# Optimization experiments

Measured on AMD Instinct MI355X. Metric: run time of the kernel, lower is better.

## Reference

```python
import jax, jax.numpy as jnp
import numpy as np

N, D, E, EDGE_DIM, HID4 = 8192, 128, 262144, 50, 32


def setup_inputs() -> dict:
    key = jax.random.key(0)
    k = jax.random.split(key, 8)
    return {
        "mag": jax.random.uniform(k[0], (N, D), dtype=jnp.float32),
        "phase": jax.random.normal(k[1], (N, D), dtype=jnp.float32),
        "edge_index": jax.random.randint(k[2], (2, E), 0, N, dtype=jnp.int64),
        "rbf": jax.random.uniform(k[3], (E, EDGE_DIM), dtype=jnp.float32),
        "W1": jax.random.normal(k[4], (EDGE_DIM, HID4), dtype=jnp.float32) * 0.1,
        "b1": jnp.zeros((HID4,), dtype=jnp.float32),
        "W2": jax.random.normal(k[5], (HID4, 1), dtype=jnp.float32) * 0.1,
        "b2": jnp.zeros((1,), dtype=jnp.float32),
    }


def reference(mag, phase, edge_index, rbf, W1, b1, W2, b2):
    # score_ij = sum_d |z_i||z_j| cos(theta_i - theta_j) / sqrt(D)
    # cos(a-b) identity: = (mag*cos(phase)) @ (mag*cos(phase))^T + (mag*sin)@(mag*sin)^T
    scale = jnp.sqrt(jnp.asarray(mag.shape[-1], mag.dtype))
    a = mag * jnp.cos(phase)  # [N, D]
    b = mag * jnp.sin(phase)  # [N, D]
    scores = (a @ a.T + b @ b.T) / scale  # [N, N]
    # edge bias: Linear -> SiLU -> Linear -> scalar, scattered onto (i, j)
    h = jax.nn.silu(rbf @ W1 + b1)       # [E, HID4]
    bias = (h @ W2 + b2)[:, 0]           # [E]
    scores = scores.at[edge_index[0], edge_index[1]].add(bias)
    attn = jax.nn.softmax(scores, axis=1)  # softmax over keys j
    new_mag = attn @ mag
    new_phase = attn @ phase
    return new_mag, new_phase
```

## Files before the change

### kernel.cpp

```cpp
#include <hip/hip_runtime.h>
#include <hip/hip_bf16.h>

#define NN 8192
#define DD 128
#define DQK 256
#define EE 262144
#define EDGE_DIM 50
#define HID 32
#define CAP 96
#define SCALE 0.08838834764831845f
#define SCALE_LOG2E 0.12752455522410585f

using f32x4 = __attribute__((ext_vector_type(4))) float;
using f32x2 = __attribute__((ext_vector_type(2))) float;
using bf16x8 = __attribute__((ext_vector_type(8))) short;
using s16x4 = __attribute__((ext_vector_type(4))) short;

static __device__ __forceinline__ short f2b(float f) {
  __hip_bfloat16 h = __float2bfloat16(f);
  return __builtin_bit_cast(short, h);
}
static __device__ __forceinline__ float b2f(short s) {
  unsigned u = ((unsigned)(unsigned short)s) << 16;
  return __builtin_bit_cast(float, u);
}
static __device__ __forceinline__ void gll(const short* g, short* l) {
  __builtin_amdgcn_global_load_lds(
      (const __attribute__((address_space(1))) void*)g,
      (__attribute__((address_space(3))) void*)l, 16, 0, 0);
}

__global__ __launch_bounds__(256) void k1_mega(
    const float* __restrict__ mag, const float* __restrict__ phase,
    short* __restrict__ qkb, short* __restrict__ vtb,
    const float* __restrict__ rbf, const float* __restrict__ W1,
    const float* __restrict__ b1, const float* __restrict__ W2,
    const float* __restrict__ b2, const int* __restrict__ eidx,
    float* __restrict__ bias, int* __restrict__ cnt, int* __restrict__ slot) {
  __shared__ float tile[64][65];
  __shared__ alignas(16) float w1s[EDGE_DIM * HID];
  __shared__ alignas(16) float b1s[HID];
  __shared__ alignas(16) float w2s[HID];
  __shared__ float b2s;
  int b = blockIdx.x;
  int tid = threadIdx.x;
  if (b < 4096) {
    int t = b * 256 + tid;
    int n = t >> 7, d = t & 127;
    float m = mag[t], p = phase[t];
    float sn, cs;
    __sincosf(p, &sn, &cs);
    qkb[(size_t)n * DQK + d] = f2b(m * cs);
    qkb[(size_t)n * DQK + 128 + d] = f2b(m * sn);
    return;
  }
  if (b < 4608) {
    int r = b - 4096;
    int bn = r & 127, bd = (r >> 7) & 1, sel = r >> 8;
    const float* src = sel ? phase : mag;
#pragma unroll
    for (int rep = 0; rep < 16; ++rep) {
      int idx = rep * 256 + tid;
      int rr = idx >> 6, c = idx & 63;
      tile[rr][c] = src[(size_t)(bn * 64 + rr) * DD + bd * 64 + c];
    }
    __syncthreads();
#pragma unroll
    for (int rep = 0; rep < 16; ++rep) {
      int idx = rep * 256 + tid;
      int rr = idx >> 6, c = idx & 63;
      vtb[(size_t)(sel * 128 + bd * 64 + rr) * NN + bn * 64 + c] = f2b(tile[c][rr]);
    }
    return;
  }
  for (int k = tid; k < EDGE_DIM * HID; k += 256) w1s[k] = W1[k];
  if (tid < HID) { b1s[tid] = b1[tid]; w2s[tid] = W2[tid]; }
  if (tid == 0) b2s = b2[0];
  __syncthreads();
  int e = (b - 4608) * 256 + tid;
  const float* rrow = rbf + (size_t)e * EDGE_DIM;
  f32x4 r4[12];
#pragma unroll
  for (int k = 0; k < 12; ++k) r4[k] = *reinterpret_cast<const f32x4*>(rrow + 4 * k);
  f32x2 rt2 = *reinterpret_cast<const f32x2*>(rrow + 48);
  f32x4 h[8];
#pragma unroll
  for (int jj = 0; jj < 8; ++jj) h[jj] = reinterpret_cast<const f32x4*>(b1s)[jj];
#pragma unroll
  for (int k = 0; k < 12; ++k) {
#pragma unroll
    for (int qq = 0; qq < 4; ++qq) {
      const f32x4* wrow = reinterpret_cast<const f32x4*>(w1s + (4 * k + qq) * HID);
#pragma unroll
      for (int jj = 0; jj < 8; ++jj) h[jj] += r4[k][qq] * wrow[jj];
    }
  }
  {
    const f32x4* w48 = reinterpret_cast<const f32x4*>(w1s + 48 * HID);
    const f32x4* w49 = reinterpret_cast<const f32x4*>(w1s + 49 * HID);
#pragma unroll
    for (int jj = 0; jj < 8; ++jj) h[jj] += rt2.x * w48[jj] + rt2.y * w49[jj];
  }
  float outv = b2s;
#pragma unroll
  for (int jj = 0; jj < 8; ++jj) {
    f32x4 x = h[jj];
    f32x4 sl;
#pragma unroll
    for (int q = 0; q < 4; ++q) sl[q] = x[q] / (1.0f + __expf(-x[q]));
    f32x4 pr = sl * reinterpret_cast<const f32x4*>(w2s)[jj];
    outv += pr.x + pr.y + pr.z + pr.w;
  }
  bias[e] = outv;
  int i = eidx[e];
  int p = atomicAdd(&cnt[i], 1);
  if (p < CAP) slot[i * CAP + p] = e;
}

constexpr int TBM = 64;
constexpr int TBN = 128;

template <int NSPLIT>
__global__ __launch_bounds__(512, 4) void k5_flash(
    const short* __restrict__ qk,
    const short* __restrict__ vt,
    float* __restrict__ nump,
    float* __restrict__ denp) {
  constexpr int QCOLS = NN / NSPLIT;
  constexpr int NCHUNK = QCOLS / TBN;
  constexpr int GPQ = 8 / NSPLIT;
  __shared__ alignas(16) short Qs[TBM * 256];
  __shared__ alignas(16) short KV[2 * TBN * 64];
  __shared__ alignas(16) short Ps[TBM * 128];
  int b = blockIdx.x;
  int q = (b & 7) / GPQ;
  int rb = (b >> 3) * GPQ + (b & (GPQ - 1));
  int tid = threadIdx.x;
  int w = tid >> 6, lane = tid & 63;
  int wr = w >> 2, wc = w & 3;
  int l15 = lane & 15, quad = lane >> 4;
  int rsw = l15 & 7;
  int wbase = w * 64;
  int r0 = rb * TBM;
  int cbase = q * QCOLS;

#pragma unroll
  for (int p = 0; p < 4; ++p) {
    int idx = p * 512 + tid;
    int row = idx >> 5, gs = idx & 31;
    gll(qk + (size_t)(r0 + row) * DQK + ((gs ^ (row & 7)) * 8),
        &Qs[(p * 512 + wbase) * 8]);
  }

  f32x4 o[2][4] = {};
  float den[2][4] = {};
  __syncthreads();

  for (int ch = 0; ch < NCHUNK; ++ch) {
    int c0 = cbase + ch * TBN;
#pragma unroll
    for (int p = 0; p < 2; ++p) {
      int idx = p * 512 + tid;
      int col = idx >> 3, gs = idx & 7;
      gll(qk + (size_t)(c0 + col) * DQK + ((gs ^ (col & 7)) * 8),
          &KV[(p * 512 + wbase) * 8]);
    }
    __syncthreads();
    f32x4 s[2][2] = {};
#pragma unroll
    for (int bk = 0; bk < 4; ++bk) {
      int buf = bk & 1;
      if (bk < 3) {
        int nb = buf ^ 1;
#pragma unroll
        for (int p = 0; p < 2; ++p) {
          int idx = p * 512 + tid;
          int col = idx >> 3, gs = idx & 7;
          gll(qk + (size_t)(c0 + col) * DQK + (bk + 1) * 64 + ((gs ^ (col & 7)) * 8),
              &KV[nb * 8192 + (p * 512 + wbase) * 8]);
        }
      }
#pragma unroll
      for (int ks = 0; ks < 2; ++ks) {
        int g = ks * 4 + quad;
        bf16x8 a[2], bb[2];
#pragma unroll
        for (int rt = 0; rt < 2; ++rt)
          a[rt] = *(const bf16x8*)&Qs[(wr * 32 + rt * 16 + l15) * 256 +
                                      ((bk * 8 + g) ^ rsw) * 8];
#pragma unroll
        for (int ct = 0; ct < 2; ++ct)
          bb[ct] = *(const bf16x8*)&KV[buf * 8192 + (wc * 32 + ct * 16 + l15) * 64 +
                                       (g ^ rsw) * 8];
#pragma unroll
        for (int rt = 0; rt < 2; ++rt)
#pragma unroll
          for (int ct = 0; ct < 2; ++ct)
            s[rt][ct] = __builtin_amdgcn_mfma_f32_16x16x32_bf16(a[rt], bb[ct],
                                                                s[rt][ct], 0, 0, 0);
      }
      __syncthreads();
    }
#pragma unroll
    for (int rt = 0; rt < 2; ++rt)
#pragma unroll
      for (int ct = 0; ct < 2; ++ct) {
        int col = wc * 32 + ct * 16 + l15;
        int cg = col >> 3, co = col & 7;
#pragma unroll
        for (int r = 0; r < 4; ++r) {
          float pv = exp2f(s[rt][ct][r] * SCALE_LOG2E);
          den[rt][r] += pv;
          int row = wr * 32 + rt * 16 + quad * 4 + r;
          Ps[row * 128 + ((cg ^ (row & 7)) * 8 + co)] = f2b(pv);
        }
      }
    __syncthreads();
#pragma unroll
    for (int jb = 0; jb < 2; ++jb) {
#pragma unroll
      for (int p = 0; p < 4; ++p) {
        int idx = p * 512 + tid;
        int feat = idx >> 3, gs = idx & 7;
        gll(vt + (size_t)feat * NN + c0 + jb * 64 + ((gs ^ (feat & 7)) * 8),
            &KV[(p * 512 + wbase) * 8]);
      }
      __syncthreads();
#pragma unroll
      for (int ks = 0; ks < 2; ++ks) {
        int g = ks * 4 + quad;
        bf16x8 pa[2], vb[4];
#pragma unroll
        for (int rt = 0; rt < 2; ++rt) {
          int row = wr * 32 + rt * 16 + l15;
          pa[rt] = *(const bf16x8*)&Ps[row * 128 +
                                       (((jb * 8 + g) ^ (row & 7)) * 8)];
        }
#pragma unroll
        for (int ft = 0; ft < 4; ++ft)
          vb[ft] = *(const bf16x8*)&KV[(wc * 64 + ft * 16 + l15) * 64 + (g ^ rsw) * 8];
#pragma unroll
        for (int rt = 0; rt < 2; ++rt)
#pragma unroll
          for (int ft = 0; ft < 4; ++ft)
            o[rt][ft] = __builtin_amdgcn_mfma_f32_16x16x32_bf16(pa[rt], vb[ft],
                                                                o[rt][ft], 0, 0, 0);
      }
      __syncthreads();
    }
  }
  float* npB = nump + (size_t)q * NN * DQK;
#pragma unroll
  for (int rt = 0; rt < 2; ++rt)
#pragma unroll
    for (int ft = 0; ft < 4; ++ft) {
      int row = r0 + wr * 32 + rt * 16 + quad * 4;
      int feat = wc * 64 + ft * 16 + l15;
#pragma unroll
      for (int r = 0; r < 4; ++r)
        npB[(size_t)(row + r) * DQK + feat] = o[rt][ft][r];
    }
  float* dl = reinterpret_cast<float*>(KV);
#pragma unroll
  for (int rt = 0; rt < 2; ++rt)
#pragma unroll
    for (int r = 0; r < 4; ++r) {
      float d = den[rt][r];
      d += __shfl_xor(d, 1);
      d += __shfl_xor(d, 2);
      d += __shfl_xor(d, 4);
      d += __shfl_xor(d, 8);
      if (l15 == 0) dl[wc * TBM + wr * 32 + rt * 16 + quad * 4 + r] = d;
    }
  __syncthreads();
  if (tid < TBM) {
    float d = dl[0 * TBM + tid] + dl[1 * TBM + tid] + dl[2 * TBM + tid] +
              dl[3 * TBM + tid];
    denp[q * NN + r0 + tid] = d;
  }
}

__global__ __launch_bounds__(256) void k6_combine(
    const int* __restrict__ eidx, const float* __restrict__ bias,
    const int* __restrict__ cntArr, const int* __restrict__ slot,
    const short* __restrict__ qk, const float* __restrict__ mag,
    const float* __restrict__ phase, const float* __restrict__ nump,
    const float* __restrict__ denp, float* __restrict__ out, int nsplit) {
  __shared__ short qs[DQK];
  __shared__ int js[CAP];
  __shared__ float bs[CAP];
  __shared__ float ess[CAP];
  __shared__ int keepf[CAP];
  __shared__ f32x4 ncl[4][64];
  __shared__ float dcl[4];
  int i = blockIdx.x;
  int tid = threadIdx.x;
  int wave = tid >> 6;
  int lane = tid & 63;
  int cnt = cntArr[i];
  if (cnt > CAP) cnt = CAP;
  if (tid < DQK) qs[tid] = qk[(size_t)i * DQK + tid];
  for (int p = tid; p < cnt; p += 256) {
    int e = slot[i * CAP + p];
    js[p] = eidx[EE + e];
    bs[p] = bias[e];
  }
  __syncthreads();
  int sub = lane & 7;
  for (int p = wave * 8 + (lane >> 3); p < cnt; p += 32) {
    int j = js[p];
    const bf16x8* kb = reinterpret_cast<const bf16x8*>(qk + (size_t)j * DQK + sub * 32);
    const bf16x8* qa = reinterpret_cast<const bf16x8*>(qs + sub * 32);
    float sp = 0.f;
#pragma unroll
    for (int t = 0; t < 4; ++t) {
      bf16x8 qv = qa[t];
      bf16x8 kv = kb[t];
#pragma unroll
      for (int u = 0; u < 8; ++u) sp += b2f(qv[u]) * b2f(kv[u]);
    }
    sp += __shfl_xor(sp, 1);
    sp += __shfl_xor(sp, 2);
    sp += __shfl_xor(sp, 4);
    if (sub == 0) ess[p] = __expf(sp * SCALE);
  }
  __syncthreads();
  {
    float bsum = 0.f;
    int keep = 0;
    if (tid < cnt) {
      int j = js[tid];
      bsum = bs[tid];
      keep = 1;
      for (int qq = 0; qq < cnt; ++qq) {
        if (qq == tid || js[qq] != j) continue;
        if (qq < tid) { keep = 0; break; }
        bsum += bs[qq];
      }
    }
    __syncthreads();
    if (tid < cnt) { bs[tid] = bsum; keepf[tid] = keep; }
    __syncthreads();
  }
  const float* vbase = (lane < 32) ? (mag + 4 * lane) : (phase + 4 * lane - 128);
  f32x4 nc = {0.f, 0.f, 0.f, 0.f};
  float denc = 0.f;
  if (wave < nsplit) {
    nc = *reinterpret_cast<const f32x4*>(nump + ((size_t)wave * NN + i) * DQK + 4 * lane);
    if (lane == 0) denc = denp[wave * NN + i];
  }
  for (int p = wave; p < cnt; p += 4) {
    if (!keepf[p]) continue;
    float delta = ess[p] * expm1f(bs[p]);
    denc += delta;
    f32x4 v = *reinterpret_cast<const f32x4*>(vbase + (size_t)js[p] * DD);
    nc += delta * v;
  }
  ncl[wave][lane] = nc;
  if (lane == 0) dcl[wave] = denc;
  __syncthreads();
  if (wave == 0) {
    f32x4 nd = ncl[0][lane] + ncl[1][lane] + ncl[2][lane] + ncl[3][lane];
    float den = dcl[0] + dcl[1] + dcl[2] + dcl[3];
    f32x4 res = nd * (1.0f / den);
    if (lane < 32)
      *reinterpret_cast<f32x4*>(out + (size_t)i * DD + 4 * lane) = res;
    else
      *reinterpret_cast<f32x4*>(out + (size_t)NN * DD + (size_t)i * DD + 4 * lane - 128) = res;
  }
}

constexpr size_t OFF_QK = 0;
constexpr size_t OFF_VT = (size_t)NN * DQK * 2;
constexpr size_t OFF_BIAS = OFF_VT + (size_t)DQK * NN * 2;
constexpr size_t OFF_CNT = OFF_BIAS + (size_t)EE * 4;
constexpr size_t OFF_SLOT = OFF_CNT + (size_t)NN * 4;
constexpr size_t OFF_NUMP = (OFF_SLOT + (size_t)NN * CAP * 4 + 255) & ~(size_t)255;
constexpr size_t WS_NEED4 = OFF_NUMP + 4ull * NN * DQK * 4 + 4ull * NN * 4;
constexpr size_t WS_NEED2 = OFF_NUMP + 2ull * NN * DQK * 4 + 2ull * NN * 4;

extern "C" void kernel_launch(void* const* d_in, const int* in_sizes, int n_in,
                              void* d_out, int out_size, void* d_ws, size_t ws_size,
                              hipStream_t stream) {
  const float* mag = (const float*)d_in[0];
  const float* phase = (const float*)d_in[1];
  const int* eidx = (const int*)d_in[2];
  const float* rbf = (const float*)d_in[3];
  const float* W1 = (const float*)d_in[4];
  const float* b1 = (const float*)d_in[5];
  const float* W2 = (const float*)d_in[6];
  const float* b2 = (const float*)d_in[7];
  float* out = (float*)d_out;
  char* ws = (char*)d_ws;
  if (ws_size < WS_NEED2) return;
  int nsplit = (ws_size >= WS_NEED4) ? 4 : 2;

  short* qkb = (short*)(ws + OFF_QK);
  short* vtb = (short*)(ws + OFF_VT);
  float* bias = (float*)(ws + OFF_BIAS);
  int* cnt = (int*)(ws + OFF_CNT);
  int* slot = (int*)(ws + OFF_SLOT);
  float* nump = (float*)(ws + OFF_NUMP);
  float* denp = (float*)(ws + OFF_NUMP + (size_t)nsplit * NN * DQK * 4);

  hipMemsetAsync(cnt, 0, (size_t)NN * 4, stream);
  k1_mega<<<5632, 256, 0, stream>>>(mag, phase, qkb, vtb, rbf, W1, b1, W2, b2,
                                    eidx, bias, cnt, slot);
  if (nsplit == 4)
    k5_flash<4><<<(NN / TBM) * 4, 512, 0, stream>>>(qkb, vtb, nump, denp);
  else
    k5_flash<2><<<(NN / TBM) * 2, 512, 0, stream>>>(qkb, vtb, nump, denp);
  k6_combine<<<NN, 256, 0, stream>>>(eidx, bias, cnt, slot, qkb, mag, phase, nump,
                                     denp, out, nsplit);
}
```

Measured before the change: 292.8 us.

## Hold Q fragments in registers and load full K/V tiles per chunk

The flash kernel now keeps each wave's Q rows as register fragments instead of staging Q in shared memory. The wave grid changes from 2x4 to 4x2, so each wave owns 16 rows and 64 key columns (128 output features). Each chunk loads the whole 128x256 K tile, and then the whole V tile, into one shared buffer in a single pass, replacing the 4-step double-buffered K loads and the 2-step V loads. This cuts the number of barriers and LDS reads of Q. In exchange it gives up the overlap between K loads and MFMA work, raises register pressure from the qf and o arrays, and changes the LDS footprint, which may affect occupancy under launch_bounds(512,4).

New measurement: 420.2 us. +43.5%, slower.

```diff
diff --git a/kernel.cpp b/kernel.cpp
--- a/kernel.cpp
+++ b/kernel.cpp
@@ -129,155 +129,111 @@
   constexpr int QCOLS = NN / NSPLIT;
   constexpr int NCHUNK = QCOLS / TBN;
   constexpr int GPQ = 8 / NSPLIT;
-  __shared__ alignas(16) short Qs[TBM * 256];
-  __shared__ alignas(16) short KV[2 * TBN * 64];
+  __shared__ alignas(16) short Kb[TBN * 256];
   __shared__ alignas(16) short Ps[TBM * 128];
   int b = blockIdx.x;
   int q = (b & 7) / GPQ;
   int rb = (b >> 3) * GPQ + (b & (GPQ - 1));
   int tid = threadIdx.x;
   int w = tid >> 6, lane = tid & 63;
-  int wr = w >> 2, wc = w & 3;
+  int wr = w >> 1, wc = w & 1;
   int l15 = lane & 15, quad = lane >> 4;
-  int rsw = l15 & 7;
   int wbase = w * 64;
   int r0 = rb * TBM;
   int cbase = q * QCOLS;
 
-#pragma unroll
-  for (int p = 0; p < 4; ++p) {
-    int idx = p * 512 + tid;
-    int row = idx >> 5, gs = idx & 31;
-    gll(qk + (size_t)(r0 + row) * DQK + ((gs ^ (row & 7)) * 8),
-        &Qs[(p * 512 + wbase) * 8]);
-  }
-
-  f32x4 o[2][4] = {};
-  float den[2][4] = {};
-  __syncthreads();
+  bf16x8 qf[8];
+  {
+    const short* qrow = qk + (size_t)(r0 + wr * 16 + l15) * DQK;
+#pragma unroll
+    for (int ks = 0; ks < 8; ++ks)
+      qf[ks] = *(const bf16x8*)(qrow + ks * 32 + quad * 8);
+  }
+
+  f32x4 o[8] = {};
+  float den[4] = {};
 
   for (int ch = 0; ch < NCHUNK; ++ch) {
     int c0 = cbase + ch * TBN;
-#pragma unroll
-    for (int p = 0; p < 2; ++p) {
+    __syncthreads();
+#pragma unroll
+    for (int p = 0; p < 8; ++p) {
       int idx = p * 512 + tid;
-      int col = idx >> 3, gs = idx & 7;
+      int col = idx >> 5, gs = idx & 31;
       gll(qk + (size_t)(c0 + col) * DQK + ((gs ^ (col & 7)) * 8),
-          &KV[(p * 512 + wbase) * 8]);
-    }
-    __syncthreads();
-    f32x4 s[2][2] = {};
-#pragma unroll
-    for (int bk = 0; bk < 4; ++bk) {
-      int buf = bk & 1;
-      if (bk < 3) {
-        int nb = buf ^ 1;
-#pragma unroll
-        for (int p = 0; p < 2; ++p) {
-          int idx = p * 512 + tid;
-          int col = idx >> 3, gs = idx & 7;
-          gll(qk + (size_t)(c0 + col) * DQK + (bk + 1) * 64 + ((gs ^ (col & 7)) * 8),
-              &KV[nb * 8192 + (p * 512 + wbase) * 8]);
-        }
+          &Kb[(p * 512 + wbase) * 8]);
+    }
+    __syncthreads();
+    f32x4 s[4] = {};
+#pragma unroll
+    for (int ks = 0; ks < 8; ++ks) {
+      int g = ks * 4 + quad;
+      bf16x8 kf[4];
+#pragma unroll
+      for (int ct = 0; ct < 4; ++ct) {
+        int col = wc * 64 + ct * 16 + l15;
+        kf[ct] = *(const bf16x8*)&Kb[col * 256 + ((g ^ (col & 7)) * 8)];
       }
 #pragma unroll
-      for (int ks = 0; ks < 2; ++ks) {
-        int g = ks * 4 + quad;
-        bf16x8 a[2], bb[2];
-#pragma unroll
-        for (int rt = 0; rt < 2; ++rt)
-          a[rt] = *(const bf16x8*)&Qs[(wr * 32 + rt * 16 + l15) * 256 +
-                                      ((bk * 8 + g) ^ rsw) * 8];
-#pragma unroll
-        for (int ct = 0; ct < 2; ++ct)
-          bb[ct] = *(const bf16x8*)&KV[buf * 8192 + (wc * 32 + ct * 16 + l15) * 64 +
-                                       (g ^ rsw) * 8];
-#pragma unroll
-        for (int rt = 0; rt < 2; ++rt)
-#pragma unroll
-          for (int ct = 0; ct < 2; ++ct)
-            s[rt][ct] = __builtin_amdgcn_mfma_f32_16x16x32_bf16(a[rt], bb[ct],
-                                                                s[rt][ct], 0, 0, 0);
+      for (int ct = 0; ct < 4; ++ct)
+        s[ct] = __builtin_amdgcn_mfma_f32_16x16x32_bf16(qf[ks], kf[ct], s[ct], 0, 0, 0);
+    }
+#pragma unroll
+    for (int ct = 0; ct < 4; ++ct) {
+      int col = wc * 64 + ct * 16 + l15;
+      int cg = col >> 3, co = col & 7;
+#pragma unroll
+      for (int r = 0; r < 4; ++r) {
+        float pv = exp2f(s[ct][r] * SCALE_LOG2E);
+        den[r] += pv;
+        int row = wr * 16 + quad * 4 + r;
+        Ps[row * 128 + ((cg ^ (row & 7)) * 8 + co)] = f2b(pv);
       }
-      __syncthreads();
-    }
-#pragma unroll
-    for (int rt = 0; rt < 2; ++rt)
-#pragma unroll
-      for (int ct = 0; ct < 2; ++ct) {
-        int col = wc * 32 + ct * 16 + l15;
-        int cg = col >> 3, co = col & 7;
-#pragma unroll
-        for (int r = 0; r < 4; ++r) {
-          float pv = exp2f(s[rt][ct][r] * SCALE_LOG2E);
-          den[rt][r] += pv;
-          int row = wr * 32 + rt * 16 + quad * 4 + r;
-          Ps[row * 128 + ((cg ^ (row & 7)) * 8 + co)] = f2b(pv);
-        }
+    }
+    __syncthreads();
+#pragma unroll
+    for (int p = 0; p < 8; ++p) {
+      int idx = p * 512 + tid;
+      int feat = idx >> 4, gs = idx & 15;
+      gll(vt + (size_t)feat * NN + c0 + ((gs ^ (feat & 7)) * 8),
+          &Kb[(p * 512 + wbase) * 8]);
+    }
+    __syncthreads();
+#pragma unroll
+    for (int ks = 0; ks < 4; ++ks) {
+      int g = ks * 4 + quad;
+      int row = wr * 16 + l15;
+      bf16x8 pa = *(const bf16x8*)&Ps[row * 128 + ((g ^ (row & 7)) * 8)];
+#pragma unroll
+      for (int ft = 0; ft < 8; ++ft) {
+        int feat = wc * 128 + ft * 16 + l15;
+        bf16x8 vb = *(const bf16x8*)&Kb[feat * 128 + ((g ^ (feat & 7)) * 8)];
+        o[ft] = __builtin_amdgcn_mfma_f32_16x16x32_bf16(pa, vb, o[ft], 0, 0, 0);
       }
-    __syncthreads();
-#pragma unroll
-    for (int jb = 0; jb < 2; ++jb) {
-#pragma unroll
-      for (int p = 0; p < 4; ++p) {
-        int idx = p * 512 + tid;
-        int feat = idx >> 3, gs = idx & 7;
-        gll(vt + (size_t)feat * NN + c0 + jb * 64 + ((gs ^ (feat & 7)) * 8),
-            &KV[(p * 512 + wbase) * 8]);
-      }
-      __syncthreads();
-#pragma unroll
-      for (int ks = 0; ks < 2; ++ks) {
-        int g = ks * 4 + quad;
-        bf16x8 pa[2], vb[4];
-#pragma unroll
-        for (int rt = 0; rt < 2; ++rt) {
-          int row = wr * 32 + rt * 16 + l15;
-          pa[rt] = *(const bf16x8*)&Ps[row * 128 +
-                                       (((jb * 8 + g) ^ (row & 7)) * 8)];
-        }
-#pragma unroll
-        for (int ft = 0; ft < 4; ++ft)
-          vb[ft] = *(const bf16x8*)&KV[(wc * 64 + ft * 16 + l15) * 64 + (g ^ rsw) * 8];
-#pragma unroll
-        for (int rt = 0; rt < 2; ++rt)
-#pragma unroll
-          for (int ft = 0; ft < 4; ++ft)
-            o[rt][ft] = __builtin_amdgcn_mfma_f32_16x16x32_bf16(pa[rt], vb[ft],
-                                                                o[rt][ft], 0, 0, 0);
-      }
-      __syncthreads();
     }
   }
   float* npB = nump + (size_t)q * NN * DQK;
 #pragma unroll
-  for (int rt = 0; rt < 2; ++rt)
-#pragma unroll
-    for (int ft = 0; ft < 4; ++ft) {
-      int row = r0 + wr * 32 + rt * 16 + quad * 4;
-      int feat = wc * 64 + ft * 16 + l15;
-#pragma unroll
-      for (int r = 0; r < 4; ++r)
-        npB[(size_t)(row + r) * DQK + feat] = o[rt][ft][r];
-    }
-  float* dl = reinterpret_cast<float*>(KV);
-#pragma unroll
-  for (int rt = 0; rt < 2; ++rt)
-#pragma unroll
-    for (int r = 0; r < 4; ++r) {
-      float d = den[rt][r];
-      d += __shfl_xor(d, 1);
-      d += __shfl_xor(d, 2);
-      d += __shfl_xor(d, 4);
-      d += __shfl_xor(d, 8);
-      if (l15 == 0) dl[wc * TBM + wr * 32 + rt * 16 + quad * 4 + r] = d;
-    }
-  __syncthreads();
-  if (tid < TBM) {
-    float d = dl[0 * TBM + tid] + dl[1 * TBM + tid] + dl[2 * TBM + tid] +
-              dl[3 * TBM + tid];
-    denp[q * NN + r0 + tid] = d;
-  }
+  for (int ft = 0; ft < 8; ++ft) {
+    int row = r0 + wr * 16 + quad * 4;
+    int feat = wc * 128 + ft * 16 + l15;
+#pragma unroll
+    for (int r = 0; r < 4; ++r)
+      npB[(size_t)(row + r) * DQK + feat] = o[ft][r];
+  }
+  __syncthreads();
+  float* dl = reinterpret_cast<float*>(Kb);
+#pragma unroll
+  for (int r = 0; r < 4; ++r) {
+    float d = den[r];
+    d += __shfl_xor(d, 1);
+    d += __shfl_xor(d, 2);
+    d += __shfl_xor(d, 4);
+    d += __shfl_xor(d, 8);
+    if (l15 == 0) dl[wc * TBM + wr * 16 + quad * 4 + r] = d;
+  }
+  __syncthreads();
+  if (tid < TBM) denp[q * NN + r0 + tid] = dl[tid] + dl[TBM + tid];
 }
 
 __global__ __launch_bounds__(256) void k6_combine(
```

## Shrink combine kernel to one wave and gather bf16 values for edge corrections

Applied to the files above, without the earlier changes.

k1 now also writes a row-major bf16 copy of mag and phase, and k6_combine gathers its sparse edge-correction value rows from that copy instead of from the fp32 inputs, halving the bytes per gathered row. The combine kernel drops from 256 to 64 threads per row. It does all per-edge work in one wave with two half-wave groups and sums the split partials in the final step. This cuts block overhead and gather traffic, but adds a bf16 write in k1 and lowers precision of the correction term.

Measured after the change: 270.5 us. -7.6%, faster.

```diff
diff --git a/kernel.cpp b/kernel.cpp
--- a/kernel.cpp
+++ b/kernel.cpp
@@ -32,7 +32,7 @@
 
 __global__ __launch_bounds__(256) void k1_mega(
     const float* __restrict__ mag, const float* __restrict__ phase,
-    short* __restrict__ qkb, short* __restrict__ vtb,
+    short* __restrict__ qkb, short* __restrict__ vtb, short* __restrict__ vb16,
     const float* __restrict__ rbf, const float* __restrict__ W1,
     const float* __restrict__ b1, const float* __restrict__ W2,
     const float* __restrict__ b2, const int* __restrict__ eidx,
@@ -52,6 +52,8 @@
     __sincosf(p, &sn, &cs);
     qkb[(size_t)n * DQK + d] = f2b(m * cs);
     qkb[(size_t)n * DQK + 128 + d] = f2b(m * sn);
+    vb16[(size_t)n * DQK + d] = f2b(m);
+    vb16[(size_t)n * DQK + 128 + d] = f2b(p);
     return;
   }
   if (b < 4608) {
@@ -280,34 +282,33 @@
   }
 }
 
-__global__ __launch_bounds__(256) void k6_combine(
+__global__ __launch_bounds__(64) void k6_combine(
     const int* __restrict__ eidx, const float* __restrict__ bias,
     const int* __restrict__ cntArr, const int* __restrict__ slot,
-    const short* __restrict__ qk, const float* __restrict__ mag,
-    const float* __restrict__ phase, const float* __restrict__ nump,
-    const float* __restrict__ denp, float* __restrict__ out, int nsplit) {
+    const short* __restrict__ qk, const short* __restrict__ vb16,
+    const float* __restrict__ nump, const float* __restrict__ denp,
+    float* __restrict__ out, int nsplit) {
   __shared__ short qs[DQK];
   __shared__ int js[CAP];
   __shared__ float bs[CAP];
   __shared__ float ess[CAP];
   __shared__ int keepf[CAP];
-  __shared__ f32x4 ncl[4][64];
-  __shared__ float dcl[4];
+  __shared__ float ncl[2][32][8];
+  __shared__ float dcl[2];
   int i = blockIdx.x;
-  int tid = threadIdx.x;
-  int wave = tid >> 6;
-  int lane = tid & 63;
+  int lane = threadIdx.x;
   int cnt = cntArr[i];
   if (cnt > CAP) cnt = CAP;
-  if (tid < DQK) qs[tid] = qk[(size_t)i * DQK + tid];
-  for (int p = tid; p < cnt; p += 256) {
+  *reinterpret_cast<s16x4*>(&qs[lane * 4]) =
+      *reinterpret_cast<const s16x4*>(qk + (size_t)i * DQK + lane * 4);
+  for (int p = lane; p < cnt; p += 64) {
     int e = slot[i * CAP + p];
     js[p] = eidx[EE + e];
     bs[p] = bias[e];
   }
   __syncthreads();
   int sub = lane & 7;
-  for (int p = wave * 8 + (lane >> 3); p < cnt; p += 32) {
+  for (int p = lane >> 3; p < cnt; p += 8) {
     int j = js[p];
     const bf16x8* kb = reinterpret_cast<const bf16x8*>(qk + (size_t)j * DQK + sub * 32);
     const bf16x8* qa = reinterpret_cast<const bf16x8*>(qs + sub * 32);
@@ -326,53 +327,74 @@
   }
   __syncthreads();
   {
-    float bsum = 0.f;
-    int keep = 0;
-    if (tid < cnt) {
-      int j = js[tid];
-      bsum = bs[tid];
-      keep = 1;
+    int myp[2];
+    float mybsum[2];
+    int mykeep[2];
+    int nm = 0;
+    for (int p = lane; p < cnt; p += 64) {
+      int j = js[p];
+      float bsum = bs[p];
+      int keep = 1;
       for (int qq = 0; qq < cnt; ++qq) {
-        if (qq == tid || js[qq] != j) continue;
-        if (qq < tid) { keep = 0; break; }
+        if (qq == p || js[qq] != j) continue;
+        if (qq < p) { keep = 0; break; }
         bsum += bs[qq];
       }
+      myp[nm] = p; mybsum[nm] = bsum; mykeep[nm] = keep; ++nm;
     }
     __syncthreads();
-    if (tid < cnt) { bs[tid] = bsum; keepf[tid] = keep; }
+    for (int k = 0; k < nm; ++k) { bs[myp[k]] = mybsum[k]; keepf[myp[k]] = mykeep[k]; }
     __syncthreads();
   }
-  const float* vbase = (lane < 32) ? (mag + 4 * lane) : (phase + 4 * lane - 128);
-  f32x4 nc = {0.f, 0.f, 0.f, 0.f};
+  int grp = lane >> 5;
+  int l31 = lane & 31;
+  f32x4 nc0 = {0.f, 0.f, 0.f, 0.f}, nc1 = {0.f, 0.f, 0.f, 0.f};
   float denc = 0.f;
-  if (wave < nsplit) {
-    nc = *reinterpret_cast<const f32x4*>(nump + ((size_t)wave * NN + i) * DQK + 4 * lane);
-    if (lane == 0) denc = denp[wave * NN + i];
-  }
-  for (int p = wave; p < cnt; p += 4) {
+  for (int p = grp; p < cnt; p += 2) {
     if (!keepf[p]) continue;
     float delta = ess[p] * expm1f(bs[p]);
     denc += delta;
-    f32x4 v = *reinterpret_cast<const f32x4*>(vbase + (size_t)js[p] * DD);
-    nc += delta * v;
-  }
-  ncl[wave][lane] = nc;
-  if (lane == 0) dcl[wave] = denc;
-  __syncthreads();
-  if (wave == 0) {
-    f32x4 nd = ncl[0][lane] + ncl[1][lane] + ncl[2][lane] + ncl[3][lane];
-    float den = dcl[0] + dcl[1] + dcl[2] + dcl[3];
-    f32x4 res = nd * (1.0f / den);
-    if (lane < 32)
-      *reinterpret_cast<f32x4*>(out + (size_t)i * DD + 4 * lane) = res;
-    else
-      *reinterpret_cast<f32x4*>(out + (size_t)NN * DD + (size_t)i * DD + 4 * lane - 128) = res;
+    bf16x8 v = *reinterpret_cast<const bf16x8*>(vb16 + (size_t)js[p] * DQK + l31 * 8);
+#pragma unroll
+    for (int u = 0; u < 4; ++u) nc0[u] += delta * b2f(v[u]);
+#pragma unroll
+    for (int u = 0; u < 4; ++u) nc1[u] += delta * b2f(v[4 + u]);
+  }
+#pragma unroll
+  for (int u = 0; u < 4; ++u) {
+    ncl[grp][l31][u] = nc0[u];
+    ncl[grp][l31][4 + u] = nc1[u];
+  }
+  if (l31 == 0) dcl[grp] = denc;
+  __syncthreads();
+  if (grp == 0) {
+    float den = dcl[0] + dcl[1];
+    f32x4 a0, a1;
+#pragma unroll
+    for (int u = 0; u < 4; ++u) {
+      a0[u] = ncl[0][l31][u] + ncl[1][l31][u];
+      a1[u] = ncl[0][l31][4 + u] + ncl[1][l31][4 + u];
+    }
+    for (int qq = 0; qq < nsplit; ++qq) {
+      const float* np = nump + ((size_t)qq * NN + i) * DQK + l31 * 8;
+      a0 += *reinterpret_cast<const f32x4*>(np);
+      a1 += *reinterpret_cast<const f32x4*>(np + 4);
+      den += denp[qq * NN + i];
+    }
+    float inv = 1.0f / den;
+    a0 *= inv;
+    a1 *= inv;
+    float* dst = (l31 < 16) ? (out + (size_t)i * DD + l31 * 8)
+                            : (out + (size_t)NN * DD + (size_t)i * DD + l31 * 8 - 128);
+    *reinterpret_cast<f32x4*>(dst) = a0;
+    *reinterpret_cast<f32x4*>(dst + 4) = a1;
   }
 }
 
 constexpr size_t OFF_QK = 0;
 constexpr size_t OFF_VT = (size_t)NN * DQK * 2;
-constexpr size_t OFF_BIAS = OFF_VT + (size_t)DQK * NN * 2;
+constexpr size_t OFF_VB16 = OFF_VT + (size_t)DQK * NN * 2;
+constexpr size_t OFF_BIAS = OFF_VB16 + (size_t)NN * DQK * 2;
 constexpr size_t OFF_CNT = OFF_BIAS + (size_t)EE * 4;
 constexpr size_t OFF_SLOT = OFF_CNT + (size_t)NN * 4;
 constexpr size_t OFF_NUMP = (OFF_SLOT + (size_t)NN * CAP * 4 + 255) & ~(size_t)255;
@@ -397,6 +419,7 @@
 
   short* qkb = (short*)(ws + OFF_QK);
   short* vtb = (short*)(ws + OFF_VT);
+  short* vb16 = (short*)(ws + OFF_VB16);
   float* bias = (float*)(ws + OFF_BIAS);
   int* cnt = (int*)(ws + OFF_CNT);
   int* slot = (int*)(ws + OFF_SLOT);
@@ -404,12 +427,12 @@
   float* denp = (float*)(ws + OFF_NUMP + (size_t)nsplit * NN * DQK * 4);
 
   hipMemsetAsync(cnt, 0, (size_t)NN * 4, stream);
-  k1_mega<<<5632, 256, 0, stream>>>(mag, phase, qkb, vtb, rbf, W1, b1, W2, b2,
-                                    eidx, bias, cnt, slot);
+  k1_mega<<<5632, 256, 0, stream>>>(mag, phase, qkb, vtb, vb16, rbf, W1, b1, W2,
+                                    b2, eidx, bias, cnt, slot);
   if (nsplit == 4)
     k5_flash<4><<<(NN / TBM) * 4, 512, 0, stream>>>(qkb, vtb, nump, denp);
   else
     k5_flash<2><<<(NN / TBM) * 2, 512, 0, stream>>>(qkb, vtb, nump, denp);
-  k6_combine<<<NN, 256, 0, stream>>>(eidx, bias, cnt, slot, qkb, mag, phase, nump,
-                                     denp, out, nsplit);
-}
+  k6_combine<<<NN, 64, 0, stream>>>(eidx, bias, cnt, slot, qkb, vb16, nump, denp,
+                                    out, nsplit);
+}
```
